# Kernel optimization log

Measured on AMD Instinct MI355X. Metric: run time of the kernel, lower is better.

Reference implementation:

```python
import jax, jax.numpy as jnp
import numpy as np

NH = 8          # num_heads (init kwarg)
NUM_GROUPS = 32
EPS = 1e-5


def setup_inputs() -> dict:
    key = jax.random.key(0)
    ks = jax.random.split(key, 4)
    B, C, H, W = 2, 512, 64, 64
    x = jax.random.normal(ks[0], (B, C, H, W), dtype=jnp.float32)
    qkv_w = jax.random.normal(ks[1], (3 * C, C), dtype=jnp.float32) * (1.0 / np.sqrt(C))
    proj_w = jax.random.normal(ks[2], (C, C), dtype=jnp.float32) * (1.0 / np.sqrt(C))
    proj_b = jax.random.normal(ks[3], (C,), dtype=jnp.float32) * 0.02
    gn_w = jnp.ones((C,), dtype=jnp.float32)
    gn_b = jnp.zeros((C,), dtype=jnp.float32)
    return {"x": x, "qkv_w": qkv_w, "proj_w": proj_w, "proj_b": proj_b,
            "gn_w": gn_w, "gn_b": gn_b}


def _group_norm(x, gamma, beta):
    B, C, H, W = x.shape
    xg = x.reshape(B, NUM_GROUPS, C // NUM_GROUPS, H, W)
    mean = xg.mean(axis=(2, 3, 4), keepdims=True)
    var = xg.var(axis=(2, 3, 4), keepdims=True)
    xg = (xg - mean) * jax.lax.rsqrt(var + EPS)
    x = xg.reshape(B, C, H, W)
    return x * gamma[None, :, None, None] + beta[None, :, None, None]


def reference(x, qkv_w, proj_w, proj_b, gn_w, gn_b):
    B, C, H, W = x.shape
    h = _group_norm(x, gn_w, gn_b)
    # 1x1 conv == channel matmul
    qkv = jnp.einsum('oc,bchw->bohw', qkv_w, h)  # [B, 3C, H, W]
    # faithful legacy reshape: per-head contiguous [q,k,v] blocks of 3*C//NH channels
    qkv = qkv.reshape(B * NH, 3 * C // NH, H * W)
    q, k, v = jnp.split(qkv, 3, axis=1)          # each [B*NH, C//NH, HW]
    scale = 1.0 / np.sqrt(np.sqrt(C // NH))
    attn = jnp.einsum('bci,bcj->bij', q * scale, k * scale)  # [B*NH, HW, HW]
    attn = jax.nn.softmax(attn, axis=-1)
    hout = jnp.einsum('bij,bcj->bci', attn, v)   # [B*NH, C//NH, HW]
    hout = hout.reshape(B, C, H, W)
    hout = jnp.einsum('oc,bchw->bohw', proj_w, hout) + proj_b[None, :, None, None]
    return x + hout
```

## Files before the change

kernel.cpp:

```cpp
#include <hip/hip_runtime.h>
#include <math.h>

typedef __attribute__((ext_vector_type(8))) short short8;
typedef __attribute__((ext_vector_type(4))) short short4v;
typedef __attribute__((ext_vector_type(4))) float floatx4;
typedef __attribute__((ext_vector_type(16))) float floatx16;

__device__ __forceinline__ unsigned short f2bf(float f) {
  union { float f; unsigned int u; } v; v.f = f;
  unsigned int r = v.u + 0x7fffu + ((v.u >> 16) & 1u);
  return (unsigned short)(r >> 16);
}

__device__ __forceinline__ unsigned int pack2(unsigned short a, unsigned short b) {
  return (unsigned int)a | ((unsigned int)b << 16);
}

__device__ __forceinline__ unsigned int rbits(float f) {
  union { float f; unsigned int u; } v; v.f = f;
  return v.u + 0x8000u;
}

__device__ __forceinline__ float fast_exp2(float x) {
#if __has_builtin(__builtin_amdgcn_exp2f)
  return __builtin_amdgcn_exp2f(x);
#else
  return exp2f(x);
#endif
}

__device__ __forceinline__ void async16(const unsigned short* gp, unsigned short* lp) {
  __builtin_amdgcn_global_load_lds(
      (__attribute__((address_space(1))) void*)(gp),
      (__attribute__((address_space(3))) void*)(lp), 16, 0, 0);
}

__global__ void gn_stats(const float* __restrict__ x, float* __restrict__ stats) {
  int bg = blockIdx.x;
  const float4* p = (const float4*)(x + (size_t)bg * 65536);
  float s = 0.f, ss = 0.f;
  for (int i = threadIdx.x; i < 16384; i += 256) {
    float4 v = p[i];
    s  += v.x + v.y + v.z + v.w;
    ss += v.x*v.x + v.y*v.y + v.z*v.z + v.w*v.w;
  }
  #pragma unroll
  for (int off = 32; off >= 1; off >>= 1) {
    s  += __shfl_xor(s,  off, 64);
    ss += __shfl_xor(ss, off, 64);
  }
  __shared__ float red[2][4];
  int wv = threadIdx.x >> 6;
  if ((threadIdx.x & 63) == 0) { red[0][wv] = s; red[1][wv] = ss; }
  __syncthreads();
  if (threadIdx.x == 0) {
    s  = red[0][0] + red[0][1] + red[0][2] + red[0][3];
    ss = red[1][0] + red[1][1] + red[1][2] + red[1][3];
    float mean = s * (1.f/65536.f);
    float var  = ss * (1.f/65536.f) - mean*mean;
    stats[2*bg]   = mean;
    stats[2*bg+1] = rsqrtf(var + 1e-5f);
  }
}

__global__ void gn_apply_t(const float* __restrict__ x, const float* __restrict__ stats,
                           const float* __restrict__ gw, const float* __restrict__ gb,
                           unsigned short* __restrict__ h_t) {
  __shared__ __align__(16) unsigned short tile[64][72];
  const int b = blockIdx.z, c0 = blockIdx.y * 64, hw0 = blockIdx.x * 64;
  const int t = threadIdx.x;
  {
    const int cl = t >> 2;
    const int hs = (t & 3) * 16;
    const int c  = c0 + cl;
    const int g  = c >> 4;
    const float mean = stats[2*(b*32 + g)];
    const float rstd = stats[2*(b*32 + g) + 1];
    const float w  = gw[c] * rstd;
    const float bb = gb[c] - mean * w;
    const float4* src = (const float4*)(x + ((size_t)(b*512 + c))*4096 + hw0 + hs);
    #pragma unroll
    for (int i = 0; i < 4; i++) {
      float4 vv = src[i];
      unsigned short* d = &tile[cl][hs + i*4];
      d[0] = f2bf(vv.x*w + bb); d[1] = f2bf(vv.y*w + bb);
      d[2] = f2bf(vv.z*w + bb); d[3] = f2bf(vv.w*w + bb);
    }
  }
  __syncthreads();
  {
    const int hwl = t >> 2;
    const int cs  = (t & 3) * 16;
    uint4 w0, w1;
    w0.x = pack2(tile[cs+ 0][hwl], tile[cs+ 1][hwl]);
    w0.y = pack2(tile[cs+ 2][hwl], tile[cs+ 3][hwl]);
    w0.z = pack2(tile[cs+ 4][hwl], tile[cs+ 5][hwl]);
    w0.w = pack2(tile[cs+ 6][hwl], tile[cs+ 7][hwl]);
    w1.x = pack2(tile[cs+ 8][hwl], tile[cs+ 9][hwl]);
    w1.y = pack2(tile[cs+10][hwl], tile[cs+11][hwl]);
    w1.z = pack2(tile[cs+12][hwl], tile[cs+13][hwl]);
    w1.w = pack2(tile[cs+14][hwl], tile[cs+15][hwl]);
    unsigned short* dst = h_t + ((size_t)(b*4096 + hw0 + hwl))*512 + c0 + cs;
    *(uint4*)dst       = w0;
    *(uint4*)(dst + 8) = w1;
  }
}

__global__ void castw2(const float* __restrict__ sa, unsigned short* __restrict__ da, int n4a,
                       const float* __restrict__ sb, unsigned short* __restrict__ db) {
  int i = blockIdx.x * 256 + threadIdx.x;
  const float* s; unsigned short* d;
  if (i < n4a) { s = sa; d = da; }
  else { i -= n4a; s = sb; d = db; }
  float4 vv = ((const float4*)s)[i];
  uint2 o;
  o.x = pack2(f2bf(vv.x), f2bf(vv.y));
  o.y = pack2(f2bf(vv.z), f2bf(vv.w));
  ((uint2*)d)[i] = o;
}

template <int MODE>
__global__ __launch_bounds__(256, 2)
void gemm_bt(const unsigned short* __restrict__ A,
             const unsigned short* __restrict__ Bt,
             unsigned short* __restrict__ q_t,
             unsigned short* __restrict__ k_t,
             unsigned short* __restrict__ v_,
             float* __restrict__ outp,
             const float* __restrict__ xres,
             const float* __restrict__ pbias) {
  __shared__ __align__(16) unsigned short As[128*32];
  __shared__ __align__(16) unsigned short Bs[128*32];
  const int b   = blockIdx.z;
  const int n0  = blockIdx.x * 128;
  const int o0  = blockIdx.y * 128;
  const int tid = threadIdx.x;
  const int wave = tid >> 6, lane = tid & 63;
  const int wr = wave >> 1, wc = wave & 1;
  const int fm = lane & 15, fq = lane >> 4;
  const int srow = lane >> 2, scol = (lane & 3) * 8;

  const unsigned short* Ab = A + (size_t)o0 * 512;
  const unsigned short* Bb = Bt + ((size_t)b*4096 + n0) * 512;

  bool vsw[4];
  #pragma unroll
  for (int fr = 0; fr < 4; fr++) {
    const int ob = o0 + wr*64 + fr*16;
    vsw[fr] = (MODE == 0) && ((ob % 192) >> 6) == 2;
  }

  floatx4 acc[4][4];
  #pragma unroll
  for (int i = 0; i < 4; i++)
    #pragma unroll
    for (int j = 0; j < 4; j++) acc[i][j] = (floatx4){0.f,0.f,0.f,0.f};

  for (int k0 = 0; k0 < 512; k0 += 32) {
    __syncthreads();
    #pragma unroll
    for (int cc = 0; cc < 2; cc++) {
      int ch = wave*2 + cc;
      async16(Ab + (size_t)(ch*16 + srow)*512 + k0 + scol, &As[ch*512]);
      async16(Bb + (size_t)(ch*16 + srow)*512 + k0 + scol, &Bs[ch*512]);
    }
    __syncthreads();
    short8 af[4], bf[4];
    #pragma unroll
    for (int f = 0; f < 4; f++) {
      af[f] = *(const short8*)&As[(wr*64 + f*16 + fm)*32 + fq*8];
      bf[f] = *(const short8*)&Bs[(wc*64 + f*16 + fm)*32 + fq*8];
    }
    #pragma unroll
    for (int fr = 0; fr < 4; fr++) {
      if (vsw[fr]) {
        #pragma unroll
        for (int fc = 0; fc < 4; fc++)
          acc[fr][fc] = __builtin_amdgcn_mfma_f32_16x16x32_bf16(bf[fc], af[fr], acc[fr][fc], 0, 0, 0);
      } else {
        #pragma unroll
        for (int fc = 0; fc < 4; fc++)
          acc[fr][fc] = __builtin_amdgcn_mfma_f32_16x16x32_bf16(af[fr], bf[fc], acc[fr][fc], 0, 0, 0);
      }
    }
  }

  if (MODE == 0) {
    #pragma unroll
    for (int fr = 0; fr < 4; fr++) {
      const int ob     = o0 + wr*64 + fr*16;
      const int head   = ob / 192;
      const int rem    = ob % 192;
      const int region = rem >> 6;
      const int bhh    = b*8 + head;
      #pragma unroll
      for (int fc = 0; fc < 4; fc++) {
        if (region == 0) {
          const int i = n0 + wc*64 + fc*16 + fm;
          const int dsub = (rem & 63) + fq*4;
          unsigned short t4[4];
          #pragma unroll
          for (int r = 0; r < 4; r++) t4[r] = f2bf(acc[fr][fc][r] * 0.18033688f);
          uint2 o; o.x = pack2(t4[0], t4[1]); o.y = pack2(t4[2], t4[3]);
          *(uint2*)&q_t[((size_t)bhh*4096 + i)*64 + dsub] = o;
        } else if (region == 1) {
          const int i = n0 + wc*64 + fc*16 + fm;
          const int dsub = (rem & 63) + fq*4;
          unsigned short t4[4];
          #pragma unroll
          for (int r = 0; r < 4; r++) t4[r] = f2bf(acc[fr][fc][r]);
          uint2 o; o.x = pack2(t4[0], t4[1]); o.y = pack2(t4[2], t4[3]);
          *(uint2*)&k_t[((size_t)bhh*4096 + i)*64 + dsub] = o;
        } else {
          const int dsub = (rem & 63) + fm;
          const int tok0 = n0 + wc*64 + fc*16 + fq*4;
          unsigned short t4[4];
          #pragma unroll
          for (int r = 0; r < 4; r++) t4[r] = f2bf(acc[fr][fc][r]);
          uint2 o; o.x = pack2(t4[0], t4[1]); o.y = pack2(t4[2], t4[3]);
          *(uint2*)&v_[((size_t)bhh*64 + dsub)*4096 + tok0] = o;
        }
      }
    }
  } else {
    #pragma unroll
    for (int fr = 0; fr < 4; fr++)
      #pragma unroll
      for (int fc = 0; fc < 4; fc++) {
        const int i = n0 + wc*64 + fc*16 + fm;
        #pragma unroll
        for (int r = 0; r < 4; r++) {
          const int o = o0 + wr*64 + fr*16 + fq*4 + r;
          const size_t idx = ((size_t)b*512 + o)*4096 + i;
          outp[idx] = xres[idx] + pbias[o] + acc[fr][fc][r];
        }
      }
  }
}

__global__ __launch_bounds__(256, 2)
void attn_kernel(const unsigned short* __restrict__ q_t,
                 const unsigned short* __restrict__ k_t,
                 const unsigned short* __restrict__ v_,
                 unsigned short* __restrict__ hout_t) {
  __shared__ __align__(16) unsigned short Ks[2][64*72];
  __shared__ __align__(16) unsigned short Vs[2][64*72];

  const int bh  = blockIdx.x;
  const int q0  = blockIdx.y * 128;
  const int tid = threadIdx.x;
  const int wave = tid >> 6, lane = tid & 63;
  const int ln = lane & 31, h = lane >> 5;

  short8 qf[4];
  {
    const unsigned short* qrow = q_t + ((size_t)bh*4096 + q0 + wave*32 + ln)*64;
    #pragma unroll
    for (int kc = 0; kc < 4; kc++)
      qf[kc] = *(const short8*)(qrow + kc*16 + h*8);
  }

  floatx16 o_acc[2];
  #pragma unroll
  for (int dn = 0; dn < 2; dn++)
    #pragma unroll
    for (int r = 0; r < 16; r++) o_acc[dn][r] = 0.f;
  float l = 0.f;

  const int sr = tid >> 3;
  const int sc = (tid & 7) * 8;
  const unsigned short* kbase = k_t + (size_t)bh*262144;
  const unsigned short* vbase = v_  + (size_t)bh*262144;

  uint4 kr0 = *(const uint4*)&kbase[(size_t)sr*64 + sc];
  uint4 kr1 = *(const uint4*)&kbase[(size_t)(sr+32)*64 + sc];
  uint4 vr0 = *(const uint4*)&vbase[(size_t)sr*4096 + sc];
  uint4 vr1 = *(const uint4*)&vbase[(size_t)(sr+32)*4096 + sc];

  for (int it = 0; it < 64; it++) {
    unsigned short* Kc = Ks[it & 1];
    unsigned short* Vc = Vs[it & 1];
    *(uint4*)&Kc[sr*72 + sc]      = kr0;
    *(uint4*)&Kc[(sr+32)*72 + sc] = kr1;
    *(uint4*)&Vc[sr*72 + sc]      = vr0;
    *(uint4*)&Vc[(sr+32)*72 + sc] = vr1;
    __syncthreads();

    {
      const int jn = ((it + 1) & 63) * 64;
      kr0 = *(const uint4*)&kbase[(size_t)(jn + sr)*64 + sc];
      kr1 = *(const uint4*)&kbase[(size_t)(jn + sr + 32)*64 + sc];
      vr0 = *(const uint4*)&vbase[(size_t)sr*4096 + jn + sc];
      vr1 = *(const uint4*)&vbase[(size_t)(sr+32)*4096 + jn + sc];
    }

    floatx16 st[2];
    #pragma unroll
    for (int mj = 0; mj < 2; mj++) {
      #pragma unroll
      for (int r = 0; r < 16; r++) st[mj][r] = 0.f;
      #pragma unroll
      for (int kc = 0; kc < 4; kc++) {
        short8 kA = *(const short8*)&Kc[(mj*32 + ln)*72 + kc*16 + h*8];
        st[mj] = __builtin_amdgcn_mfma_f32_32x32x16_bf16(kA, qf[kc], st[mj], 0, 0, 0);
      }
    }

    unsigned pk[2][8];
    #pragma unroll
    for (int mj = 0; mj < 2; mj++) {
      #pragma unroll
      for (int rp = 0; rp < 8; rp++) {
        float p0 = fast_exp2(st[mj][2*rp]);
        float p1 = fast_exp2(st[mj][2*rp + 1]);
        l += p0 + p1;
        pk[mj][rp] = __builtin_amdgcn_perm(rbits(p1), rbits(p0), 0x07060302u);
      }
    }

    #pragma unroll
    for (int mj = 0; mj < 2; mj++) {
      #pragma unroll
      for (int t = 0; t < 4; t++) {
        union { unsigned u[2]; short4v s; } uu;
        uu.u[0] = pk[mj][2*t]; uu.u[1] = pk[mj][2*t + 1];
        const short4v af = uu.s;
        #pragma unroll
        for (int dn = 0; dn < 2; dn++) {
          const short4v vf = *(const short4v*)&Vc[(dn*32 + ln)*72 + mj*32 + t*8 + h*4];
          o_acc[dn] = __builtin_amdgcn_mfma_f32_32x32x8bf16_1k(af, vf, o_acc[dn], 0, 0, 0);
        }
      }
    }
  }

  l += __shfl_xor(l, 32, 64);
  const float linv = 1.f / l;

  const int bb = bh >> 3;
  const int cb = (bh & 7) * 64;
  #pragma unroll
  for (int r = 0; r < 16; r++) {
    const int il = (r & 3) + 8*(r >> 2) + 4*h;
    const float inv = __shfl(linv, il, 64);
    const int i = q0 + wave*32 + il;
    unsigned short* dst = &hout_t[((size_t)bb*4096 + i)*512 + cb + ln];
    dst[0]  = f2bf(o_acc[0][r] * inv);
    dst[32] = f2bf(o_acc[1][r] * inv);
  }
}

extern "C" void kernel_launch(void* const* d_in, const int* in_sizes, int n_in,
                              void* d_out, int out_size, void* d_ws, size_t ws_size,
                              hipStream_t stream) {
  (void)in_sizes; (void)n_in; (void)out_size; (void)ws_size;
  const float* x      = (const float*)d_in[0];
  const float* qkv_w  = (const float*)d_in[1];
  const float* proj_w = (const float*)d_in[2];
  const float* proj_b = (const float*)d_in[3];
  const float* gn_w   = (const float*)d_in[4];
  const float* gn_b   = (const float*)d_in[5];
  float* out = (float*)d_out;

  char* ws = (char*)d_ws;
  unsigned short* h_t   = (unsigned short*)(ws);
  unsigned short* q_t   = (unsigned short*)(ws + ((size_t)8  << 20));
  unsigned short* k_t   = (unsigned short*)(ws + ((size_t)16 << 20));
  unsigned short* v_    = (unsigned short*)(ws + ((size_t)24 << 20));
  unsigned short* wqkv  = (unsigned short*)(ws + ((size_t)32 << 20));
  unsigned short* wproj = (unsigned short*)(ws + ((size_t)34 << 20));
  float* stats          = (float*)(ws + ((size_t)35 << 20));
  unsigned short* hout_t = h_t;

  gn_stats<<<dim3(64), dim3(256), 0, stream>>>(x, stats);
  gn_apply_t<<<dim3(64, 8, 2), dim3(256), 0, stream>>>(x, stats, gn_w, gn_b, h_t);
  castw2<<<dim3(1024), dim3(256), 0, stream>>>(qkv_w, wqkv, 196608, proj_w, wproj);
  gemm_bt<0><<<dim3(32, 12, 2), dim3(256), 0, stream>>>(wqkv, h_t, q_t, k_t, v_,
                                                        nullptr, nullptr, nullptr);
  attn_kernel<<<dim3(16, 32), dim3(256), 0, stream>>>(q_t, k_t, v_, hout_t);
  gemm_bt<1><<<dim3(32, 4, 2), dim3(256), 0, stream>>>(wproj, hout_t,
                                                       nullptr, nullptr, nullptr,
                                                       out, x, proj_b);
}
```

Before: 233.4 us.

## Split attention over key dimension into two partial passes with a combine kernel

The attention kernel now splits the 4096 keys into two halves via blockIdx.z. Each half writes unnormalized bf16 partial outputs and row sums to workspace, and a new combine kernel adds them, normalizes, and writes hout. This doubles the grid from 512 to 1024 blocks to improve CU occupancy, with launch bounds raised to 4 blocks per CU. The V tile is also stored to LDS in a permuted layout so the PV stage can read one 8-wide vector in place of two 4-wide loads, and the QK and PV stages are interleaved per 32-key chunk. The costs are an extra kernel launch, the partial-result traffic, and bf16 rounding of the partial sums. The split path only runs when the workspace is large enough.

Result: no change. 232.9 us (-0.2%).

```diff
diff --git a/kernel.cpp b/kernel.cpp
--- a/kernel.cpp
+++ b/kernel.cpp
@@ -10,6 +10,11 @@
   union { float f; unsigned int u; } v; v.f = f;
   unsigned int r = v.u + 0x7fffu + ((v.u >> 16) & 1u);
   return (unsigned short)(r >> 16);
+}
+
+__device__ __forceinline__ float bf2f(unsigned short h) {
+  union { unsigned int u; float f; } v; v.u = ((unsigned int)h) << 16;
+  return v.f;
 }
 
 __device__ __forceinline__ unsigned int pack2(unsigned short a, unsigned short b) {
@@ -238,16 +243,22 @@
   }
 }
 
-__global__ __launch_bounds__(256, 2)
+template <int SPLIT>
+__global__ __launch_bounds__(256, 4)
 void attn_kernel(const unsigned short* __restrict__ q_t,
                  const unsigned short* __restrict__ k_t,
                  const unsigned short* __restrict__ v_,
-                 unsigned short* __restrict__ hout_t) {
+                 unsigned short* __restrict__ hout_t,
+                 unsigned short* __restrict__ o_part,
+                 float* __restrict__ l_part) {
   __shared__ __align__(16) unsigned short Ks[2][64*72];
   __shared__ __align__(16) unsigned short Vs[2][64*72];
 
   const int bh  = blockIdx.x;
   const int q0  = blockIdx.y * 128;
+  const int js  = SPLIT ? blockIdx.z : 0;
+  const int nit = SPLIT ? 32 : 64;
+  const int jbase = js * 2048;
   const int tid = threadIdx.x;
   const int wave = tid >> 6, lane = tid & 63;
   const int ln = lane & 31, h = lane >> 5;
@@ -260,100 +271,144 @@
       qf[kc] = *(const short8*)(qrow + kc*16 + h*8);
   }
 
+  const floatx16 z16 = {0.f,0.f,0.f,0.f,0.f,0.f,0.f,0.f,
+                        0.f,0.f,0.f,0.f,0.f,0.f,0.f,0.f};
   floatx16 o_acc[2];
-  #pragma unroll
-  for (int dn = 0; dn < 2; dn++)
-    #pragma unroll
-    for (int r = 0; r < 16; r++) o_acc[dn][r] = 0.f;
+  o_acc[0] = z16; o_acc[1] = z16;
   float l = 0.f;
 
   const int sr = tid >> 3;
   const int sc = (tid & 7) * 8;
+  const int c  = tid & 7;
+  const int vpos = ((c >> 2) * 32) + ((c & 3) * 4);
   const unsigned short* kbase = k_t + (size_t)bh*262144;
   const unsigned short* vbase = v_  + (size_t)bh*262144;
 
-  uint4 kr0 = *(const uint4*)&kbase[(size_t)sr*64 + sc];
-  uint4 kr1 = *(const uint4*)&kbase[(size_t)(sr+32)*64 + sc];
-  uint4 vr0 = *(const uint4*)&vbase[(size_t)sr*4096 + sc];
-  uint4 vr1 = *(const uint4*)&vbase[(size_t)(sr+32)*4096 + sc];
-
-  for (int it = 0; it < 64; it++) {
+  uint4 kr0 = *(const uint4*)&kbase[(size_t)(jbase + sr)*64 + sc];
+  uint4 kr1 = *(const uint4*)&kbase[(size_t)(jbase + sr + 32)*64 + sc];
+  uint4 vr0 = *(const uint4*)&vbase[(size_t)sr*4096 + jbase + sc];
+  uint4 vr1 = *(const uint4*)&vbase[(size_t)(sr+32)*4096 + jbase + sc];
+
+  for (int it = 0; it < nit; it++) {
     unsigned short* Kc = Ks[it & 1];
     unsigned short* Vc = Vs[it & 1];
     *(uint4*)&Kc[sr*72 + sc]      = kr0;
     *(uint4*)&Kc[(sr+32)*72 + sc] = kr1;
-    *(uint4*)&Vc[sr*72 + sc]      = vr0;
-    *(uint4*)&Vc[(sr+32)*72 + sc] = vr1;
+    *(uint2*)&Vc[sr*72 + vpos]           = *(const uint2*)&vr0;
+    *(uint2*)&Vc[sr*72 + vpos + 16]      = *((const uint2*)&vr0 + 1);
+    *(uint2*)&Vc[(sr+32)*72 + vpos]      = *(const uint2*)&vr1;
+    *(uint2*)&Vc[(sr+32)*72 + vpos + 16] = *((const uint2*)&vr1 + 1);
     __syncthreads();
 
     {
-      const int jn = ((it + 1) & 63) * 64;
+      const int jn = jbase + (((it + 1) & (nit - 1)) * 64);
       kr0 = *(const uint4*)&kbase[(size_t)(jn + sr)*64 + sc];
       kr1 = *(const uint4*)&kbase[(size_t)(jn + sr + 32)*64 + sc];
       vr0 = *(const uint4*)&vbase[(size_t)sr*4096 + jn + sc];
       vr1 = *(const uint4*)&vbase[(size_t)(sr+32)*4096 + jn + sc];
     }
 
-    floatx16 st[2];
     #pragma unroll
     for (int mj = 0; mj < 2; mj++) {
+      floatx16 st;
+      {
+        short8 kA = *(const short8*)&Kc[(mj*32 + ln)*72 + h*8];
+        st = __builtin_amdgcn_mfma_f32_32x32x16_bf16(kA, qf[0], z16, 0, 0, 0);
+      }
       #pragma unroll
-      for (int r = 0; r < 16; r++) st[mj][r] = 0.f;
-      #pragma unroll
-      for (int kc = 0; kc < 4; kc++) {
+      for (int kc = 1; kc < 4; kc++) {
         short8 kA = *(const short8*)&Kc[(mj*32 + ln)*72 + kc*16 + h*8];
-        st[mj] = __builtin_amdgcn_mfma_f32_32x32x16_bf16(kA, qf[kc], st[mj], 0, 0, 0);
-      }
-    }
-
-    unsigned pk[2][8];
-    #pragma unroll
-    for (int mj = 0; mj < 2; mj++) {
+        st = __builtin_amdgcn_mfma_f32_32x32x16_bf16(kA, qf[kc], st, 0, 0, 0);
+      }
+
+      unsigned pk[8];
       #pragma unroll
       for (int rp = 0; rp < 8; rp++) {
-        float p0 = fast_exp2(st[mj][2*rp]);
-        float p1 = fast_exp2(st[mj][2*rp + 1]);
+        float p0 = fast_exp2(st[2*rp]);
+        float p1 = fast_exp2(st[2*rp + 1]);
         l += p0 + p1;
-        pk[mj][rp] = __builtin_amdgcn_perm(rbits(p1), rbits(p0), 0x07060302u);
-      }
-    }
-
-    #pragma unroll
-    for (int mj = 0; mj < 2; mj++) {
+        pk[rp] = __builtin_amdgcn_perm(rbits(p1), rbits(p0), 0x07060302u);
+      }
+
       #pragma unroll
-      for (int t = 0; t < 4; t++) {
-        union { unsigned u[2]; short4v s; } uu;
-        uu.u[0] = pk[mj][2*t]; uu.u[1] = pk[mj][2*t + 1];
-        const short4v af = uu.s;
+      for (int t2 = 0; t2 < 2; t2++) {
+        union { unsigned u[2]; short4v s; } a0, a1;
+        a0.u[0] = pk[4*t2];     a0.u[1] = pk[4*t2 + 1];
+        a1.u[0] = pk[4*t2 + 2]; a1.u[1] = pk[4*t2 + 3];
         #pragma unroll
         for (int dn = 0; dn < 2; dn++) {
-          const short4v vf = *(const short4v*)&Vc[(dn*32 + ln)*72 + mj*32 + t*8 + h*4];
-          o_acc[dn] = __builtin_amdgcn_mfma_f32_32x32x8bf16_1k(af, vf, o_acc[dn], 0, 0, 0);
+          short8 vv = *(const short8*)&Vc[(dn*32 + ln)*72 + mj*32 + h*16 + t2*8];
+          short4v vlo = __builtin_shufflevector(vv, vv, 0, 1, 2, 3);
+          short4v vhi = __builtin_shufflevector(vv, vv, 4, 5, 6, 7);
+          o_acc[dn] = __builtin_amdgcn_mfma_f32_32x32x8bf16_1k(a0.s, vlo, o_acc[dn], 0, 0, 0);
+          o_acc[dn] = __builtin_amdgcn_mfma_f32_32x32x8bf16_1k(a1.s, vhi, o_acc[dn], 0, 0, 0);
         }
       }
     }
   }
 
   l += __shfl_xor(l, 32, 64);
-  const float linv = 1.f / l;
-
+
+  if (SPLIT) {
+    unsigned short* op = o_part + (((size_t)(js*16 + bh)*4096 + q0 + wave*32) * 64);
+    #pragma unroll
+    for (int r = 0; r < 16; r++) {
+      const int il = (r & 3) + 8*(r >> 2) + 4*h;
+      op[(size_t)il*64 + ln]      = f2bf(o_acc[0][r]);
+      op[(size_t)il*64 + 32 + ln] = f2bf(o_acc[1][r]);
+    }
+    if (lane < 32)
+      l_part[(size_t)(js*16 + bh)*4096 + q0 + wave*32 + lane] = l;
+  } else {
+    const float linv = 1.f / l;
+    const int bb = bh >> 3;
+    const int cb = (bh & 7) * 64;
+    #pragma unroll
+    for (int r = 0; r < 16; r++) {
+      const int il = (r & 3) + 8*(r >> 2) + 4*h;
+      const float inv = __shfl(linv, il, 64);
+      const int i = q0 + wave*32 + il;
+      unsigned short* dst = &hout_t[((size_t)bb*4096 + i)*512 + cb + ln];
+      dst[0]  = f2bf(o_acc[0][r] * inv);
+      dst[32] = f2bf(o_acc[1][r] * inv);
+    }
+  }
+}
+
+__global__ void attn_combine(const unsigned short* __restrict__ o_part,
+                             const float* __restrict__ l_part,
+                             unsigned short* __restrict__ hout_t) {
+  const int bh = blockIdx.x;
+  const int i0 = blockIdx.y * 64;
+  const int t  = threadIdx.x;
+  const int d4 = (t & 15) * 4;
+  const int il = t >> 4;
   const int bb = bh >> 3;
   const int cb = (bh & 7) * 64;
+  const size_t JS = (size_t)16 * 4096 * 64;
   #pragma unroll
-  for (int r = 0; r < 16; r++) {
-    const int il = (r & 3) + 8*(r >> 2) + 4*h;
-    const float inv = __shfl(linv, il, 64);
-    const int i = q0 + wave*32 + il;
-    unsigned short* dst = &hout_t[((size_t)bb*4096 + i)*512 + cb + ln];
-    dst[0]  = f2bf(o_acc[0][r] * inv);
-    dst[32] = f2bf(o_acc[1][r] * inv);
+  for (int p = 0; p < 4; p++) {
+    const int i = i0 + p*16 + il;
+    const size_t ob = ((size_t)bh*4096 + i)*64 + d4;
+    uint2 a = *(const uint2*)&o_part[ob];
+    uint2 b = *(const uint2*)&o_part[ob + JS];
+    const size_t lb = (size_t)bh*4096 + i;
+    const float inv = 1.f / (l_part[lb] + l_part[lb + 65536]);
+    float o0 = (bf2f((unsigned short)(a.x & 0xffff)) + bf2f((unsigned short)(b.x & 0xffff))) * inv;
+    float o1 = (bf2f((unsigned short)(a.x >> 16))    + bf2f((unsigned short)(b.x >> 16)))    * inv;
+    float o2 = (bf2f((unsigned short)(a.y & 0xffff)) + bf2f((unsigned short)(b.y & 0xffff))) * inv;
+    float o3 = (bf2f((unsigned short)(a.y >> 16))    + bf2f((unsigned short)(b.y >> 16)))    * inv;
+    uint2 w;
+    w.x = pack2(f2bf(o0), f2bf(o1));
+    w.y = pack2(f2bf(o2), f2bf(o3));
+    *(uint2*)&hout_t[((size_t)bb*4096 + i)*512 + cb + d4] = w;
   }
 }
 
 extern "C" void kernel_launch(void* const* d_in, const int* in_sizes, int n_in,
                               void* d_out, int out_size, void* d_ws, size_t ws_size,
                               hipStream_t stream) {
-  (void)in_sizes; (void)n_in; (void)out_size; (void)ws_size;
+  (void)in_sizes; (void)n_in; (void)out_size;
   const float* x      = (const float*)d_in[0];
   const float* qkv_w  = (const float*)d_in[1];
   const float* proj_w = (const float*)d_in[2];
@@ -370,14 +425,25 @@
   unsigned short* wqkv  = (unsigned short*)(ws + ((size_t)32 << 20));
   unsigned short* wproj = (unsigned short*)(ws + ((size_t)34 << 20));
   float* stats          = (float*)(ws + ((size_t)35 << 20));
+  unsigned short* o_part = (unsigned short*)(ws + ((size_t)36 << 20));
+  float* l_part          = (float*)(ws + ((size_t)52 << 20));
   unsigned short* hout_t = h_t;
+
+  const bool split = ws_size >= (((size_t)52 << 20) + ((size_t)1 << 19));
 
   gn_stats<<<dim3(64), dim3(256), 0, stream>>>(x, stats);
   gn_apply_t<<<dim3(64, 8, 2), dim3(256), 0, stream>>>(x, stats, gn_w, gn_b, h_t);
   castw2<<<dim3(1024), dim3(256), 0, stream>>>(qkv_w, wqkv, 196608, proj_w, wproj);
   gemm_bt<0><<<dim3(32, 12, 2), dim3(256), 0, stream>>>(wqkv, h_t, q_t, k_t, v_,
                                                         nullptr, nullptr, nullptr);
-  attn_kernel<<<dim3(16, 32), dim3(256), 0, stream>>>(q_t, k_t, v_, hout_t);
+  if (split) {
+    attn_kernel<1><<<dim3(16, 32, 2), dim3(256), 0, stream>>>(q_t, k_t, v_, nullptr,
+                                                              o_part, l_part);
+    attn_combine<<<dim3(16, 64), dim3(256), 0, stream>>>(o_part, l_part, hout_t);
+  } else {
+    attn_kernel<0><<<dim3(16, 32), dim3(256), 0, stream>>>(q_t, k_t, v_, hout_t,
+                                                           nullptr, nullptr);
+  }
   gemm_bt<1><<<dim3(32, 4, 2), dim3(256), 0, stream>>>(wproj, hout_t,
                                                        nullptr, nullptr, nullptr,
                                                        out, x, proj_b);
```
